# Performance work log

Hardware: AMD Instinct MI355X
Metric: run time of the kernel (lower is better)

Reference implementation:

```python
import jax, jax.numpy as jnp
import numpy as np

B, L, D, E, R, NMOD = 8, 2048, 4096, 4, 8, 7

def setup_inputs() -> dict:
    key = jax.random.key(0)
    ks = jax.random.split(key, 8)
    return {
        "x": jax.random.normal(ks[0], (B, L, D), dtype=jnp.float32) * 0.02,
        "expert_scores": jax.random.uniform(ks[1], (B, E), dtype=jnp.float32),
        "W_base": jax.random.normal(ks[2], (D, D), dtype=jnp.float32) * 0.02,
        "b_base": jnp.zeros((D,), dtype=jnp.float32),
        "gating_W": jax.random.normal(ks[3], (D, D), dtype=jnp.float32) * 0.02,
        "W_r": jax.random.normal(ks[4], (NMOD, D), dtype=jnp.float32) * 0.02,
        "lora_A": jax.random.normal(ks[5], (E, R, D), dtype=jnp.float32) * 0.02,
        "lora_B": jax.random.normal(ks[6], (E, D, R), dtype=jnp.float32) * 0.02,
        "module_idx": 0,
        "k": 2,
    }

def _gate_weights(expert_scores, module_prob, k, dtype):
    # rank experts by their random score (descending); Top-K -> weight 1/K
    order = jnp.argsort(-expert_scores, axis=-1)           # [B, E]
    rank = jnp.argsort(order, axis=-1)                     # [B, E] rank of each expert
    k_lo = max(1, k // 2)
    w_hi = (rank < k).astype(dtype) / k                    # prob > 0.5 branch
    w_lo = (rank < k_lo).astype(dtype) / k_lo              # prob <= 0.5 branch
    return jnp.where((module_prob > 0.5)[:, None], w_hi, w_lo)  # [B, E]

def reference(x, expert_scores, W_base, b_base, gating_W, W_r, lora_A, lora_B, module_idx, k):
    # Pooler: last token representation
    pooled = x[:, -1, :]                                   # [B, D]
    # Router: softmax(g(h) W_r) -> per-module probability
    gated = pooled @ gating_W.T                            # [B, D]
    logits = gated @ W_r.T                                 # [B, NMOD]
    probs = jax.nn.softmax(logits, axis=-1)
    module_prob = probs[:, module_idx]                     # [B]
    gate = _gate_weights(expert_scores, module_prob, k, x.dtype)  # [B, E]
    # Base linear projection
    base = x @ W_base.T + b_base                           # [B, L, D]
    # LoRA experts: sum_e gate[b,e] * (x @ A_e^T) @ B_e^T
    t = jnp.einsum('bli,eri->belr', x, lora_A)             # [B, E, L, R]
    lora = jnp.einsum('belr,eor,be->blo', t, lora_B, gate) # [B, L, D]
    return base + lora
```

## Files before the change

### kernel.cpp

```cpp
#include <hip/hip_runtime.h>
#include <hip/hip_bf16.h>


typedef short short8 __attribute__((ext_vector_type(8)));
typedef float f32x4v __attribute__((ext_vector_type(4)));

#define M_DIM 16384
#define N_DIM 4096
#define K_DIM 4160
#define D_DIM 4096
#define NGRP 130

__device__ __forceinline__ unsigned short f2b(float f) {
  unsigned u = __builtin_bit_cast(unsigned, f);
  return (unsigned short)((u + 0x7FFFu + ((u >> 16) & 1u)) >> 16);
}
__device__ __forceinline__ void async_copy16(void* lds, const void* g) {
  __builtin_amdgcn_global_load_lds(
      (const __attribute__((address_space(1))) void*)g,
      (__attribute__((address_space(3))) void*)lds, 16, 0, 0);
}
__device__ __forceinline__ short8 frag_ld(const short* base, int row, int ks, int hi, int lo) {
  return *(const short8*)(&base[row * 64 + (((ks * 4 + hi) ^ (lo & 7)) * 8)]);
}

__global__ __launch_bounds__(256) void cvt_x_k(const float* __restrict__ x,
                                               short* __restrict__ xa) {
  size_t idx = (size_t)blockIdx.x * 256 + threadIdx.x;
  size_t row = idx / 520;
  int cc = (int)(idx % 520);
  short8 o;
  if (cc < 512) {
    const float* src = x + row * (size_t)D_DIM + (size_t)cc * 8;
    float4 a = *(const float4*)(src);
    float4 b = *(const float4*)(src + 4);
    o[0] = (short)f2b(a.x); o[1] = (short)f2b(a.y);
    o[2] = (short)f2b(a.z); o[3] = (short)f2b(a.w);
    o[4] = (short)f2b(b.x); o[5] = (short)f2b(b.y);
    o[6] = (short)f2b(b.z); o[7] = (short)f2b(b.w);
  } else {
#pragma unroll
    for (int t = 0; t < 8; ++t) o[t] = 0;
  }
  *(short8*)(xa + row * (size_t)K_DIM + (size_t)cc * 8) = o;
}

__global__ __launch_bounds__(256) void cvt_w_la_k(const float* __restrict__ Wb,
                                                  const float* __restrict__ lB,
                                                  const float* __restrict__ lA,
                                                  short* __restrict__ wa,
                                                  short* __restrict__ lAb) {
  if (blockIdx.x < 8320) {
    size_t idx = (size_t)blockIdx.x * 256 + threadIdx.x;
    size_t row = idx / 520;
    int cc = (int)(idx % 520);
    short8 o;
    if (cc < 512) {
      const float* src = Wb + row * (size_t)D_DIM + (size_t)cc * 8;
      float4 a = *(const float4*)(src);
      float4 b = *(const float4*)(src + 4);
      o[0] = (short)f2b(a.x); o[1] = (short)f2b(a.y);
      o[2] = (short)f2b(a.z); o[3] = (short)f2b(a.w);
      o[4] = (short)f2b(b.x); o[5] = (short)f2b(b.y);
      o[6] = (short)f2b(b.z); o[7] = (short)f2b(b.w);
    } else if (cc < 516) {
      int e = cc - 512;
      const float* src = lB + (size_t)e * (D_DIM * 8) + row * 8;
      float4 a = *(const float4*)(src);
      float4 b = *(const float4*)(src + 4);
      o[0] = (short)f2b(a.x); o[1] = (short)f2b(a.y);
      o[2] = (short)f2b(a.z); o[3] = (short)f2b(a.w);
      o[4] = (short)f2b(b.x); o[5] = (short)f2b(b.y);
      o[6] = (short)f2b(b.z); o[7] = (short)f2b(b.w);
    } else {
#pragma unroll
      for (int t = 0; t < 8; ++t) o[t] = 0;
    }
    *(short8*)(wa + row * (size_t)K_DIM + (size_t)cc * 8) = o;
  } else {
    size_t i = (size_t)(blockIdx.x - 8320) * 256 + threadIdx.x;
    const float* s = lA + i * 8;
    float4 a = *(const float4*)s;
    float4 b = *(const float4*)(s + 4);
    short8 o;
    o[0] = (short)f2b(a.x); o[1] = (short)f2b(a.y);
    o[2] = (short)f2b(a.z); o[3] = (short)f2b(a.w);
    o[4] = (short)f2b(b.x); o[5] = (short)f2b(b.y);
    o[6] = (short)f2b(b.z); o[7] = (short)f2b(b.w);
    *(short8*)(lAb + i * 8) = o;
  }
}

__global__ __launch_bounds__(256) void gated_k(const float* __restrict__ x,
                                               const float* __restrict__ gW,
                                               float* __restrict__ gated) {
  const int j = blockIdx.x;
  const int tid = threadIdx.x;
  float acc[8];
#pragma unroll
  for (int b = 0; b < 8; ++b) acc[b] = 0.f;
  const float* w = gW + (size_t)j * D_DIM;
  for (int i = tid * 4; i < D_DIM; i += 1024) {
    float4 wv = *(const float4*)(w + i);
#pragma unroll
    for (int b = 0; b < 8; ++b) {
      const float* p = x + ((size_t)b * 2048 + 2047) * D_DIM + i;
      float4 pv = *(const float4*)p;
      acc[b] += wv.x * pv.x + wv.y * pv.y + wv.z * pv.z + wv.w * pv.w;
    }
  }
  __shared__ float red[8][4];
  const int lane = tid & 63, wv_ = tid >> 6;
#pragma unroll
  for (int b = 0; b < 8; ++b) {
    float v = acc[b];
    v += __shfl_down(v, 32); v += __shfl_down(v, 16); v += __shfl_down(v, 8);
    v += __shfl_down(v, 4);  v += __shfl_down(v, 2);  v += __shfl_down(v, 1);
    if (lane == 0) red[b][wv_] = v;
  }
  __syncthreads();
  if (tid < 8)
    gated[(size_t)tid * D_DIM + j] = red[tid][0] + red[tid][1] + red[tid][2] + red[tid][3];
}

__global__ void gate_k(const float* __restrict__ gated, const float* __restrict__ Wr,
                       const float* __restrict__ scores, const int* __restrict__ midx_p,
                       const int* __restrict__ kp, float* __restrict__ gate) {
  const int lane = threadIdx.x;
  float acc[56];
#pragma unroll
  for (int t = 0; t < 56; ++t) acc[t] = 0.f;
  for (int i = lane * 4; i < D_DIM; i += 256) {
    float4 g[8]; float4 w[7];
#pragma unroll
    for (int b = 0; b < 8; ++b) g[b] = *(const float4*)(gated + (size_t)b * D_DIM + i);
#pragma unroll
    for (int m = 0; m < 7; ++m) w[m] = *(const float4*)(Wr + (size_t)m * D_DIM + i);
#pragma unroll
    for (int m = 0; m < 7; ++m)
#pragma unroll
      for (int b = 0; b < 8; ++b)
        acc[m * 8 + b] += w[m].x * g[b].x + w[m].y * g[b].y + w[m].z * g[b].z + w[m].w * g[b].w;
  }
  __shared__ float Ls[56];
#pragma unroll
  for (int t = 0; t < 56; ++t) {
    float v = acc[t];
    v += __shfl_xor(v, 1); v += __shfl_xor(v, 2); v += __shfl_xor(v, 4);
    v += __shfl_xor(v, 8); v += __shfl_xor(v, 16); v += __shfl_xor(v, 32);
    if (lane == t) Ls[t] = v;
  }
  __syncthreads();
  if (lane < 8) {
    const int b = lane;
    float mx = -1e30f;
    for (int m = 0; m < 7; ++m) mx = fmaxf(mx, Ls[m * 8 + b]);
    float s = 0.f;
    for (int m = 0; m < 7; ++m) s += expf(Ls[m * 8 + b] - mx);
    const int mi = midx_p[0];
    const float mp = expf(Ls[mi * 8 + b] - mx) / s;
    int kv = kp[0]; if (kv < 1) kv = 1;
    int klo = kv >> 1; if (klo < 1) klo = 1;
    float sc[4];
#pragma unroll
    for (int e = 0; e < 4; ++e) sc[e] = scores[b * 4 + e];
#pragma unroll
    for (int e = 0; e < 4; ++e) {
      int rank = 0;
#pragma unroll
      for (int e2 = 0; e2 < 4; ++e2)
        rank += (sc[e2] > sc[e] || (sc[e2] == sc[e] && e2 < e)) ? 1 : 0;
      float wv = (mp > 0.5f) ? ((rank < kv) ? 1.0f / (float)kv : 0.f)
                             : ((rank < klo) ? 1.0f / (float)klo : 0.f);
      gate[b * 4 + e] = wv;
    }
  }
}

__global__ __launch_bounds__(256) void lora_t_k(const short* __restrict__ XA,
                                                const short* __restrict__ LAb,
                                                const float* __restrict__ gate,
                                                short* __restrict__ xa_w) {
  __shared__ short As[4][2048];
  __shared__ short Bs[4][2048];
  const int tid = threadIdx.x, lane = tid & 63, wave = tid >> 6;
  const int lo = lane & 15, hi = lane >> 4;
  const int wr = (wave >> 1) * 16;
  const int wc = (wave & 1) * 16;
  const size_t row0 = (size_t)blockIdx.x * 32;
  const int srow = tid >> 3;
  const int sslot = (tid & 7) ^ (srow & 7);
  const short* gA = XA + (row0 + srow) * (size_t)K_DIM + sslot * 8;
  const short* gB = LAb + (size_t)srow * D_DIM + sslot * 8;
  f32x4v acc = {};

#define LSTAGE(g)                                                              \
  async_copy16((char*)&As[(g) & 3][0] + wave * 1024, gA + (size_t)(g) * 64);   \
  async_copy16((char*)&Bs[(g) & 3][0] + wave * 1024, gB + (size_t)(g) * 64);

  LSTAGE(0)
  LSTAGE(1)
  asm volatile("s_waitcnt vmcnt(2)" ::: "memory");
  __builtin_amdgcn_s_barrier();

  for (int g = 0; g < 64; ++g) {
    const short* Atile = &As[g & 3][0];
    const short* Btile = &Bs[g & 3][0];
    short8 a0 = frag_ld(Atile, wr + lo, 0, hi, lo);
    short8 a1 = frag_ld(Atile, wr + lo, 1, hi, lo);
    short8 b0 = frag_ld(Btile, wc + lo, 0, hi, lo);
    short8 b1 = frag_ld(Btile, wc + lo, 1, hi, lo);
    acc = __builtin_amdgcn_mfma_f32_16x16x32_bf16(a0, b0, acc, 0, 0, 0);
    acc = __builtin_amdgcn_mfma_f32_16x16x32_bf16(a1, b1, acc, 0, 0, 0);
    if (g < 62) {
      LSTAGE(g + 2)
      asm volatile("s_waitcnt vmcnt(2)" ::: "memory");
    } else {
      asm volatile("s_waitcnt vmcnt(0)" ::: "memory");
    }
    __builtin_amdgcn_s_barrier();
  }

  const int b = (int)(row0 >> 11);
  const int col = wc + lo;
  const float gv = gate[b * 4 + (col >> 3)];
#pragma unroll
  for (int j = 0; j < 4; ++j) {
    const size_t r = row0 + wr + hi * 4 + j;
    xa_w[r * (size_t)K_DIM + 4096 + col] = (short)f2b(acc[j] * gv);
  }
#undef LSTAGE
}

__global__ __launch_bounds__(512, 2) void gemm_k(const short* __restrict__ A,
                                                 const short* __restrict__ B,
                                                 const float* __restrict__ bias,
                                                 float* __restrict__ C) {
  __shared__ short As[5][8192];
  __shared__ short Bs[5][8192];
  const int tid = threadIdx.x;
  const int lane = tid & 63;
  const int wave = tid >> 6;
  const int wm = wave >> 2;
  const int wn = wave & 3;
  const int lo = lane & 15, hi = lane >> 4;

  const int wg = (blockIdx.x & 7) * 128 + (blockIdx.x >> 3);
  const int brow = wg >> 4;
  const int bcol = wg & 15;

  const int srow = tid >> 2;
  const int schunk = (tid & 3) ^ ((tid >> 3) & 3);
  const short* srcA = A + (size_t)(brow * 256 + srow) * K_DIM + schunk * 8;
  const short* srcB = B + (size_t)(bcol * 256 + srow) * K_DIM + schunk * 8;
  char* ldsA0 = (char*)(&As[0][0]) + wave * 1024;
  char* ldsB0 = (char*)(&Bs[0][0]) + wave * 1024;

  const int csw = (hi ^ ((lo >> 1) & 3)) * 8;
  const int aro = (wm * 128 + lo) * 32 + csw;
  const int bro = (wn * 64 + lo) * 32 + csw;

  float bz[4];
#pragma unroll
  for (int ni = 0; ni < 4; ++ni)
    bz[ni] = bias[bcol * 256 + wn * 64 + ni * 16 + lo];

  f32x4v acc[8][4] = {};

#define STAGE_A(koff, ss)                                                      \
  async_copy16(ldsA0 + (ss) * 16384, srcA + (koff));                           \
  async_copy16(ldsA0 + (ss) * 16384 + 8192, srcA + (size_t)128 * K_DIM + (koff));
#define STAGE_B(koff, ss)                                                      \
  async_copy16(ldsB0 + (ss) * 16384, srcB + (koff));                           \
  async_copy16(ldsB0 + (ss) * 16384 + 8192, srcB + (size_t)128 * K_DIM + (koff));

#define GROUP(s, ko, sw)                                                       \
  {                                                                            \
    const short* Aslot = &As[0][0] + (s) * 8192;                               \
    const short* Bslot = &Bs[0][0] + (s) * 8192;                               \
    short8 afr[4], afr2[4], bfr[4];                                            \
    _Pragma("unroll")                                                          \
    for (int mi = 0; mi < 4; ++mi)                                             \
      afr[mi] = *(const short8*)(&Aslot[aro + mi * 512]);                      \
    _Pragma("unroll")                                                          \
    for (int ni = 0; ni < 4; ++ni)                                             \
      bfr[ni] = *(const short8*)(&Bslot[bro + ni * 512]);                      \
    _Pragma("unroll")                                                          \
    for (int mi = 0; mi < 4; ++mi)                                             \
      afr2[mi] = *(const short8*)(&Aslot[aro + 2048 + mi * 512]);              \
    __builtin_amdgcn_s_setprio(1);                                             \
    _Pragma("unroll")                                                          \
    for (int mi = 0; mi < 4; ++mi)                                             \
      _Pragma("unroll")                                                        \
      for (int ni = 0; ni < 4; ++ni)                                           \
        acc[mi][ni] = __builtin_amdgcn_mfma_f32_16x16x32_bf16(                 \
            afr[mi], bfr[ni], acc[mi][ni], 0, 0, 0);                           \
    __builtin_amdgcn_s_setprio(0);                                             \
    STAGE_A((ko), (sw));                                                       \
    STAGE_B((ko), (sw));                                                       \
    __builtin_amdgcn_s_setprio(1);                                             \
    _Pragma("unroll")                                                          \
    for (int mi = 0; mi < 4; ++mi)                                             \
      _Pragma("unroll")                                                        \
      for (int ni = 0; ni < 4; ++ni)                                           \
        acc[mi + 4][ni] = __builtin_amdgcn_mfma_f32_16x16x32_bf16(             \
            afr2[mi], bfr[ni], acc[mi + 4][ni], 0, 0, 0);                      \
    __builtin_amdgcn_s_setprio(0);                                             \
  }

  STAGE_A(0, 0);  STAGE_B(0, 0);
  STAGE_A(32, 1); STAGE_B(32, 1);
  STAGE_A(64, 2); STAGE_B(64, 2);
  asm volatile("s_waitcnt vmcnt(4)" ::: "memory");
  __builtin_amdgcn_s_barrier();

  int s0 = 0;
  for (int p = 0; p < 65; ++p) {
    const int g0 = 2 * p, g1 = g0 + 1;
    const int s1  = (s0 + 1 == 5) ? 0 : s0 + 1;
    const int sw0 = (s0 + 3 >= 5) ? s0 - 2 : s0 + 3;
    const int sw1 = (sw0 + 1 == 5) ? 0 : sw0 + 1;
    const size_t ko0 = (size_t)((g0 + 3 <= NGRP - 1) ? g0 + 3 : g0 - 2) * 32;
    const size_t ko1 = (size_t)((g1 + 3 <= NGRP - 1) ? g1 + 3 : g1 - 2) * 32;

    GROUP(s0, ko0, sw0)
    GROUP(s1, ko1, sw1)

    asm volatile("s_waitcnt vmcnt(4)" ::: "memory");
    __builtin_amdgcn_s_barrier();
    s0 = (s0 + 2 >= 5) ? s0 - 3 : s0 + 2;
  }
  asm volatile("s_waitcnt vmcnt(0)" ::: "memory");

#pragma unroll
  for (int mi = 0; mi < 8; ++mi) {
#pragma unroll
    for (int ni = 0; ni < 4; ++ni) {
      const int r0 = brow * 256 + wm * 128 + mi * 16 + hi * 4;
      const int c0 = bcol * 256 + wn * 64 + ni * 16 + lo;
#pragma unroll
      for (int j = 0; j < 4; ++j)
        C[(size_t)(r0 + j) * N_DIM + c0] = acc[mi][ni][j] + bz[ni];
    }
  }
#undef GROUP
#undef STAGE_A
#undef STAGE_B
}

extern "C" void kernel_launch(void* const* d_in, const int* in_sizes, int n_in,
                              void* d_out, int out_size, void* d_ws, size_t ws_size,
                              hipStream_t stream) {
  const float* x      = (const float*)d_in[0];
  const float* scores = (const float*)d_in[1];
  const float* Wb     = (const float*)d_in[2];
  const float* bb     = (const float*)d_in[3];
  const float* gW     = (const float*)d_in[4];
  const float* Wr     = (const float*)d_in[5];
  const float* lA     = (const float*)d_in[6];
  const float* lB     = (const float*)d_in[7];
  const int*   midx   = (const int*)d_in[8];
  const int*   kk     = (const int*)d_in[9];
  float* out = (float*)d_out;

  char* ws = (char*)d_ws;
  short* xa    = (short*)ws;
  short* wa    = (short*)(ws + 136314880u);
  float* gated = (float*)(ws + 136314880u + 34078720u);
  float* gate  = (float*)(ws + 136314880u + 34078720u + 131072u);
  short* lAb   = (short*)(ws + 136314880u + 34078720u + 131072u + 128u);

  cvt_x_k<<<33280, 256, 0, stream>>>(x, xa);
  cvt_w_la_k<<<8384, 256, 0, stream>>>(Wb, lB, lA, wa, lAb);
  gated_k<<<4096, 256, 0, stream>>>(x, gW, gated);
  gate_k<<<1, 64, 0, stream>>>(gated, Wr, scores, midx, kk, gate);
  lora_t_k<<<512, 256, 0, stream>>>(xa, lAb, gate, xa);
  gemm_k<<<1024, 512, 0, stream>>>(xa, wa, bb, out);
}
```

Measured before the change: 696.4 us.

## Fuse conversion and gating kernels into one prep launch; compute gate inside LoRA kernel

Merges the x conversion, weight/LoRA conversion and gated-projection kernels into a single block-indexed prep kernel, and drops the single-block gate kernel by having each LoRA block compute its own batch's router logits, softmax and top-k gate. This cuts three kernel launches and the serial tail of the one-block gate kernel. In exchange, each of the 512 LoRA blocks redundantly reads the gated row and Wr, adding per-block work and extra barriers.

Result: faster. 654.3 us, median of 2 (-6.0%).

```diff
diff --git a/kernel.cpp b/kernel.cpp
--- a/kernel.cpp
+++ b/kernel.cpp
@@ -23,166 +23,101 @@
 __device__ __forceinline__ short8 frag_ld(const short* base, int row, int ks, int hi, int lo) {
   return *(const short8*)(&base[row * 64 + (((ks * 4 + hi) ^ (lo & 7)) * 8)]);
 }
-
-__global__ __launch_bounds__(256) void cvt_x_k(const float* __restrict__ x,
-                                               short* __restrict__ xa) {
-  size_t idx = (size_t)blockIdx.x * 256 + threadIdx.x;
-  size_t row = idx / 520;
-  int cc = (int)(idx % 520);
+__device__ __forceinline__ short8 cvt8(const float* src) {
+  float4 a = *(const float4*)(src);
+  float4 b = *(const float4*)(src + 4);
   short8 o;
-  if (cc < 512) {
-    const float* src = x + row * (size_t)D_DIM + (size_t)cc * 8;
-    float4 a = *(const float4*)(src);
-    float4 b = *(const float4*)(src + 4);
-    o[0] = (short)f2b(a.x); o[1] = (short)f2b(a.y);
-    o[2] = (short)f2b(a.z); o[3] = (short)f2b(a.w);
-    o[4] = (short)f2b(b.x); o[5] = (short)f2b(b.y);
-    o[6] = (short)f2b(b.z); o[7] = (short)f2b(b.w);
-  } else {
-#pragma unroll
-    for (int t = 0; t < 8; ++t) o[t] = 0;
-  }
-  *(short8*)(xa + row * (size_t)K_DIM + (size_t)cc * 8) = o;
-}
-
-__global__ __launch_bounds__(256) void cvt_w_la_k(const float* __restrict__ Wb,
-                                                  const float* __restrict__ lB,
-                                                  const float* __restrict__ lA,
-                                                  short* __restrict__ wa,
-                                                  short* __restrict__ lAb) {
-  if (blockIdx.x < 8320) {
-    size_t idx = (size_t)blockIdx.x * 256 + threadIdx.x;
+  o[0] = (short)f2b(a.x); o[1] = (short)f2b(a.y);
+  o[2] = (short)f2b(a.z); o[3] = (short)f2b(a.w);
+  o[4] = (short)f2b(b.x); o[5] = (short)f2b(b.y);
+  o[6] = (short)f2b(b.z); o[7] = (short)f2b(b.w);
+  return o;
+}
+
+__global__ __launch_bounds__(256) void prep_k(const float* __restrict__ x,
+                                              const float* __restrict__ Wb,
+                                              const float* __restrict__ lB,
+                                              const float* __restrict__ lA,
+                                              const float* __restrict__ gW,
+                                              short* __restrict__ xa,
+                                              short* __restrict__ wa,
+                                              short* __restrict__ lAb,
+                                              float* __restrict__ gated) {
+  __shared__ float red[8][4];
+  const unsigned bid = blockIdx.x;
+  const int tid = threadIdx.x;
+  if (bid < 33280u) {
+    size_t idx = (size_t)bid * 256 + tid;
     size_t row = idx / 520;
     int cc = (int)(idx % 520);
     short8 o;
     if (cc < 512) {
-      const float* src = Wb + row * (size_t)D_DIM + (size_t)cc * 8;
-      float4 a = *(const float4*)(src);
-      float4 b = *(const float4*)(src + 4);
-      o[0] = (short)f2b(a.x); o[1] = (short)f2b(a.y);
-      o[2] = (short)f2b(a.z); o[3] = (short)f2b(a.w);
-      o[4] = (short)f2b(b.x); o[5] = (short)f2b(b.y);
-      o[6] = (short)f2b(b.z); o[7] = (short)f2b(b.w);
+      o = cvt8(x + row * (size_t)D_DIM + (size_t)cc * 8);
+    } else {
+#pragma unroll
+      for (int t = 0; t < 8; ++t) o[t] = 0;
+    }
+    *(short8*)(xa + row * (size_t)K_DIM + (size_t)cc * 8) = o;
+  } else if (bid < 41600u) {
+    size_t idx = (size_t)(bid - 33280u) * 256 + tid;
+    size_t row = idx / 520;
+    int cc = (int)(idx % 520);
+    short8 o;
+    if (cc < 512) {
+      o = cvt8(Wb + row * (size_t)D_DIM + (size_t)cc * 8);
     } else if (cc < 516) {
       int e = cc - 512;
-      const float* src = lB + (size_t)e * (D_DIM * 8) + row * 8;
-      float4 a = *(const float4*)(src);
-      float4 b = *(const float4*)(src + 4);
-      o[0] = (short)f2b(a.x); o[1] = (short)f2b(a.y);
-      o[2] = (short)f2b(a.z); o[3] = (short)f2b(a.w);
-      o[4] = (short)f2b(b.x); o[5] = (short)f2b(b.y);
-      o[6] = (short)f2b(b.z); o[7] = (short)f2b(b.w);
+      o = cvt8(lB + (size_t)e * (D_DIM * 8) + row * 8);
     } else {
 #pragma unroll
       for (int t = 0; t < 8; ++t) o[t] = 0;
     }
     *(short8*)(wa + row * (size_t)K_DIM + (size_t)cc * 8) = o;
+  } else if (bid < 41664u) {
+    size_t i = (size_t)(bid - 41600u) * 256 + tid;
+    *(short8*)(lAb + i * 8) = cvt8(lA + i * 8);
   } else {
-    size_t i = (size_t)(blockIdx.x - 8320) * 256 + threadIdx.x;
-    const float* s = lA + i * 8;
-    float4 a = *(const float4*)s;
-    float4 b = *(const float4*)(s + 4);
-    short8 o;
-    o[0] = (short)f2b(a.x); o[1] = (short)f2b(a.y);
-    o[2] = (short)f2b(a.z); o[3] = (short)f2b(a.w);
-    o[4] = (short)f2b(b.x); o[5] = (short)f2b(b.y);
-    o[6] = (short)f2b(b.z); o[7] = (short)f2b(b.w);
-    *(short8*)(lAb + i * 8) = o;
-  }
-}
-
-__global__ __launch_bounds__(256) void gated_k(const float* __restrict__ x,
-                                               const float* __restrict__ gW,
-                                               float* __restrict__ gated) {
-  const int j = blockIdx.x;
-  const int tid = threadIdx.x;
-  float acc[8];
-#pragma unroll
-  for (int b = 0; b < 8; ++b) acc[b] = 0.f;
-  const float* w = gW + (size_t)j * D_DIM;
-  for (int i = tid * 4; i < D_DIM; i += 1024) {
-    float4 wv = *(const float4*)(w + i);
+    const int j = (int)(bid - 41664u);
+    float acc[8];
+#pragma unroll
+    for (int b = 0; b < 8; ++b) acc[b] = 0.f;
+    const float* w = gW + (size_t)j * D_DIM;
+    for (int i = tid * 4; i < D_DIM; i += 1024) {
+      float4 wv = *(const float4*)(w + i);
+#pragma unroll
+      for (int b = 0; b < 8; ++b) {
+        const float* p = x + ((size_t)b * 2048 + 2047) * D_DIM + i;
+        float4 pv = *(const float4*)p;
+        acc[b] += wv.x * pv.x + wv.y * pv.y + wv.z * pv.z + wv.w * pv.w;
+      }
+    }
+    const int lane = tid & 63, wv_ = tid >> 6;
 #pragma unroll
     for (int b = 0; b < 8; ++b) {
-      const float* p = x + ((size_t)b * 2048 + 2047) * D_DIM + i;
-      float4 pv = *(const float4*)p;
-      acc[b] += wv.x * pv.x + wv.y * pv.y + wv.z * pv.z + wv.w * pv.w;
-    }
-  }
-  __shared__ float red[8][4];
-  const int lane = tid & 63, wv_ = tid >> 6;
-#pragma unroll
-  for (int b = 0; b < 8; ++b) {
-    float v = acc[b];
-    v += __shfl_down(v, 32); v += __shfl_down(v, 16); v += __shfl_down(v, 8);
-    v += __shfl_down(v, 4);  v += __shfl_down(v, 2);  v += __shfl_down(v, 1);
-    if (lane == 0) red[b][wv_] = v;
-  }
-  __syncthreads();
-  if (tid < 8)
-    gated[(size_t)tid * D_DIM + j] = red[tid][0] + red[tid][1] + red[tid][2] + red[tid][3];
-}
-
-__global__ void gate_k(const float* __restrict__ gated, const float* __restrict__ Wr,
-                       const float* __restrict__ scores, const int* __restrict__ midx_p,
-                       const int* __restrict__ kp, float* __restrict__ gate) {
-  const int lane = threadIdx.x;
-  float acc[56];
-#pragma unroll
-  for (int t = 0; t < 56; ++t) acc[t] = 0.f;
-  for (int i = lane * 4; i < D_DIM; i += 256) {
-    float4 g[8]; float4 w[7];
-#pragma unroll
-    for (int b = 0; b < 8; ++b) g[b] = *(const float4*)(gated + (size_t)b * D_DIM + i);
-#pragma unroll
-    for (int m = 0; m < 7; ++m) w[m] = *(const float4*)(Wr + (size_t)m * D_DIM + i);
-#pragma unroll
-    for (int m = 0; m < 7; ++m)
-#pragma unroll
-      for (int b = 0; b < 8; ++b)
-        acc[m * 8 + b] += w[m].x * g[b].x + w[m].y * g[b].y + w[m].z * g[b].z + w[m].w * g[b].w;
-  }
-  __shared__ float Ls[56];
-#pragma unroll
-  for (int t = 0; t < 56; ++t) {
-    float v = acc[t];
-    v += __shfl_xor(v, 1); v += __shfl_xor(v, 2); v += __shfl_xor(v, 4);
-    v += __shfl_xor(v, 8); v += __shfl_xor(v, 16); v += __shfl_xor(v, 32);
-    if (lane == t) Ls[t] = v;
-  }
-  __syncthreads();
-  if (lane < 8) {
-    const int b = lane;
-    float mx = -1e30f;
-    for (int m = 0; m < 7; ++m) mx = fmaxf(mx, Ls[m * 8 + b]);
-    float s = 0.f;
-    for (int m = 0; m < 7; ++m) s += expf(Ls[m * 8 + b] - mx);
-    const int mi = midx_p[0];
-    const float mp = expf(Ls[mi * 8 + b] - mx) / s;
-    int kv = kp[0]; if (kv < 1) kv = 1;
-    int klo = kv >> 1; if (klo < 1) klo = 1;
-    float sc[4];
-#pragma unroll
-    for (int e = 0; e < 4; ++e) sc[e] = scores[b * 4 + e];
-#pragma unroll
-    for (int e = 0; e < 4; ++e) {
-      int rank = 0;
-#pragma unroll
-      for (int e2 = 0; e2 < 4; ++e2)
-        rank += (sc[e2] > sc[e] || (sc[e2] == sc[e] && e2 < e)) ? 1 : 0;
-      float wv = (mp > 0.5f) ? ((rank < kv) ? 1.0f / (float)kv : 0.f)
-                             : ((rank < klo) ? 1.0f / (float)klo : 0.f);
-      gate[b * 4 + e] = wv;
-    }
+      float v = acc[b];
+      v += __shfl_down(v, 32); v += __shfl_down(v, 16); v += __shfl_down(v, 8);
+      v += __shfl_down(v, 4);  v += __shfl_down(v, 2);  v += __shfl_down(v, 1);
+      if (lane == 0) red[b][wv_] = v;
+    }
+    __syncthreads();
+    if (tid < 8)
+      gated[(size_t)tid * D_DIM + j] = red[tid][0] + red[tid][1] + red[tid][2] + red[tid][3];
   }
 }
 
 __global__ __launch_bounds__(256) void lora_t_k(const short* __restrict__ XA,
                                                 const short* __restrict__ LAb,
-                                                const float* __restrict__ gate,
+                                                const float* __restrict__ gated,
+                                                const float* __restrict__ Wr,
+                                                const float* __restrict__ scores,
+                                                const int* __restrict__ midx_p,
+                                                const int* __restrict__ kp,
                                                 short* __restrict__ xa_w) {
   __shared__ short As[4][2048];
   __shared__ short Bs[4][2048];
+  __shared__ float Lp[4][7];
+  __shared__ float Ls[7];
+  __shared__ float gateS[4];
   const int tid = threadIdx.x, lane = tid & 63, wave = tid >> 6;
   const int lo = lane & 15, hi = lane >> 4;
   const int wr = (wave >> 1) * 16;
@@ -221,9 +156,57 @@
     __builtin_amdgcn_s_barrier();
   }
 
-  const int b = (int)(row0 >> 11);
+  const int bblk = (int)(row0 >> 11);
+  {
+    float ac7[7];
+#pragma unroll
+    for (int m = 0; m < 7; ++m) ac7[m] = 0.f;
+    const float* gb = gated + (size_t)bblk * D_DIM;
+    for (int i = tid * 4; i < D_DIM; i += 1024) {
+      float4 g4 = *(const float4*)(gb + i);
+#pragma unroll
+      for (int m = 0; m < 7; ++m) {
+        float4 w4 = *(const float4*)(Wr + (size_t)m * D_DIM + i);
+        ac7[m] += w4.x * g4.x + w4.y * g4.y + w4.z * g4.z + w4.w * g4.w;
+      }
+    }
+#pragma unroll
+    for (int m = 0; m < 7; ++m) {
+      float v = ac7[m];
+      v += __shfl_xor(v, 1); v += __shfl_xor(v, 2); v += __shfl_xor(v, 4);
+      v += __shfl_xor(v, 8); v += __shfl_xor(v, 16); v += __shfl_xor(v, 32);
+      if (lane == m) Lp[wave][m] = v;
+    }
+    __syncthreads();
+    if (tid < 7) Ls[tid] = Lp[0][tid] + Lp[1][tid] + Lp[2][tid] + Lp[3][tid];
+    __syncthreads();
+    if (tid == 0) {
+      float mx = -1e30f;
+      for (int m = 0; m < 7; ++m) mx = fmaxf(mx, Ls[m]);
+      float s = 0.f;
+      for (int m = 0; m < 7; ++m) s += expf(Ls[m] - mx);
+      const int mi = midx_p[0];
+      const float mp = expf(Ls[mi] - mx) / s;
+      int kv = kp[0]; if (kv < 1) kv = 1;
+      int klo = kv >> 1; if (klo < 1) klo = 1;
+      float sc[4];
+#pragma unroll
+      for (int e = 0; e < 4; ++e) sc[e] = scores[bblk * 4 + e];
+#pragma unroll
+      for (int e = 0; e < 4; ++e) {
+        int rank = 0;
+#pragma unroll
+        for (int e2 = 0; e2 < 4; ++e2)
+          rank += (sc[e2] > sc[e] || (sc[e2] == sc[e] && e2 < e)) ? 1 : 0;
+        gateS[e] = (mp > 0.5f) ? ((rank < kv) ? 1.0f / (float)kv : 0.f)
+                               : ((rank < klo) ? 1.0f / (float)klo : 0.f);
+      }
+    }
+    __syncthreads();
+  }
+
   const int col = wc + lo;
-  const float gv = gate[b * 4 + (col >> 3)];
+  const float gv = gateS[col >> 3];
 #pragma unroll
   for (int j = 0; j < 4; ++j) {
     const size_t r = row0 + wr + hi * 4 + j;
@@ -367,13 +350,9 @@
   short* xa    = (short*)ws;
   short* wa    = (short*)(ws + 136314880u);
   float* gated = (float*)(ws + 136314880u + 34078720u);
-  float* gate  = (float*)(ws + 136314880u + 34078720u + 131072u);
   short* lAb   = (short*)(ws + 136314880u + 34078720u + 131072u + 128u);
 
-  cvt_x_k<<<33280, 256, 0, stream>>>(x, xa);
-  cvt_w_la_k<<<8384, 256, 0, stream>>>(Wb, lB, lA, wa, lAb);
-  gated_k<<<4096, 256, 0, stream>>>(x, gW, gated);
-  gate_k<<<1, 64, 0, stream>>>(gated, Wr, scores, midx, kk, gate);
-  lora_t_k<<<512, 256, 0, stream>>>(xa, lAb, gate, xa);
+  prep_k<<<45760, 256, 0, stream>>>(x, Wb, lB, lA, gW, xa, wa, lAb, gated);
+  lora_t_k<<<512, 256, 0, stream>>>(xa, lAb, gated, Wr, scores, midx, kk, xa);
   gemm_k<<<1024, 512, 0, stream>>>(xa, wa, bb, out);
 }
```
